# Kernel optimization log

Hardware: AMD Instinct MI355X
Metric: run time of the kernel (lower is better)

## Reference

```python
import jax, jax.numpy as jnp
import numpy as np

B, S, D = 8, 1024, 512
H, DH, OUT = 8, 64, 512
EPS = 1e-6

def _ln(x, scale, bias):
    m = jnp.mean(x, -1, keepdims=True)
    v = jnp.mean(jnp.square(x - m), -1, keepdims=True)
    return (x - m) * jax.lax.rsqrt(v + EPS) * scale + bias

def _rel_shift(x):
    # TransformerXL relative shift: [B,H,Q,P] -> [B,H,Q,P]
    b, h, q, p = x.shape
    x = jnp.pad(x, ((0, 0), (0, 0), (0, 0), (1, 0)))
    x = x.reshape(b, h, p + 1, q)
    return x[:, :, 1:, :].reshape(b, h, q, p)

def _gate(x, y, wry, wrx, wzy, wzx, why, whx, bg):
    # GTrXL GRU-style gating
    r = jax.nn.sigmoid(y @ wry + x @ wrx)
    z = jax.nn.sigmoid(y @ wzy + x @ wzx - bg)
    h = jnp.tanh(y @ why + (r * x) @ whx)
    return (1 - z) * x + z * h

def setup_inputs() -> dict:
    key = jax.random.key(0)
    ks = jax.random.split(key, 40)
    w = lambda k, shp: (0.02 * jax.random.normal(k, shp, jnp.float32))
    inp = {
        'values_keys': jax.random.normal(ks[0], (B, S, D), jnp.float32),
        'queries': jax.random.normal(ks[1], (B, S, D), jnp.float32),
        'pos_embed': jax.random.normal(ks[2], (S, D), jnp.float32),
        'mask': jnp.tril(jnp.ones((S, S), bool))[None, None],
        'ln1_scale': jnp.ones((D,), jnp.float32), 'ln1_bias': jnp.zeros((D,), jnp.float32),
        'wq': w(ks[3], (D, H, DH)), 'bq': jnp.zeros((H, DH), jnp.float32),
        'wk': w(ks[4], (D, H, DH)), 'bk': jnp.zeros((H, DH), jnp.float32),
        'wv': w(ks[5], (D, H, DH)), 'bv': jnp.zeros((H, DH), jnp.float32),
        'wr': w(ks[6], (D, H, DH)),
        'u_bias': w(ks[7], (H, DH)), 'v_bias': w(ks[8], (H, DH)),
        'wo': w(ks[9], (H, DH, OUT)), 'bo': jnp.zeros((OUT,), jnp.float32),
        'ln2_scale': jnp.ones((OUT,), jnp.float32), 'ln2_bias': jnp.zeros((OUT,), jnp.float32),
        'w1': w(ks[10], (OUT, OUT)), 'b1': jnp.zeros((OUT,), jnp.float32),
        'w2': w(ks[11], (OUT, OUT)), 'b2': jnp.zeros((OUT,), jnp.float32),
    }
    for gi, base in ((1, 12), (2, 19)):
        for j, nm in enumerate(['wry', 'wrx', 'wzy', 'wzx', 'why', 'whx']):
            inp['g%d_%s' % (gi, nm)] = w(ks[base + j], (OUT, OUT))
        inp['g%d_bg' % gi] = 2.0 * jnp.ones((OUT,), jnp.float32)
    return inp

def reference(values_keys, queries, pos_embed, mask, ln1_scale, ln1_bias, wq, bq, wk, bk, wv, bv, wr, u_bias, v_bias, wo, bo, ln2_scale, ln2_bias, w1, b1, w2, b2, g1_wry, g1_wrx, g1_wzy, g1_wzx, g1_why, g1_whx, g1_bg, g2_wry, g2_wrx, g2_wzy, g2_wzx, g2_why, g2_whx, g2_bg):
    vk = _ln(values_keys, ln1_scale, ln1_bias)
    qn = _ln(queries, ln1_scale, ln1_bias)
    q = jnp.einsum('bsd,dhk->bshk', qn, wq) + bq
    k = jnp.einsum('bsd,dhk->bshk', vk, wk) + bk
    v = jnp.einsum('bsd,dhk->bshk', vk, wv) + bv
    r = jnp.einsum('pd,dhk->phk', pos_embed, wr)
    ac = jnp.einsum('bqhk,bshk->bhqs', q + u_bias, k)
    bd = _rel_shift(jnp.einsum('bqhk,phk->bhqp', q + v_bias, r))
    scores = (ac + bd) * jnp.float32(1.0 / np.sqrt(DH))
    scores = jnp.where(mask, scores, jnp.float32(-1e9))
    attn = jax.nn.softmax(scores, axis=-1)
    o = jnp.einsum('bhqs,bshk->bqhk', attn, v)
    attn_out = jnp.einsum('bqhk,hko->bqo', o, wo) + bo
    out_attention = _gate(queries, jax.nn.relu(attn_out), g1_wry, g1_wrx, g1_wzy, g1_wzx, g1_why, g1_whx, g1_bg)
    h = _ln(out_attention, ln2_scale, ln2_bias)
    h = jax.nn.gelu(h @ w1 + b1) @ w2 + b2
    return _gate(h, jax.nn.relu(out_attention), g2_wry, g2_wrx, g2_wzy, g2_wzx, g2_why, g2_whx, g2_bg)
```

## Files before the change

kernel.cpp:

```cpp
#include <hip/hip_runtime.h>
#include <hip/hip_bf16.h>
#include <math.h>

#define TPB 256
#define B_   8
#define S_   1024
#define D_   512
#define H_   8
#define DH_  64
#define MTOK (B_ * S_)
#define NEL  (MTOK * D_)
#define WMAT (D_ * D_)

typedef __attribute__((ext_vector_type(8))) short bf8;
typedef __attribute__((ext_vector_type(4))) float f4;

__device__ __forceinline__ float ld_any(const void* p, long i, bool bf) {
  if (bf) {
    unsigned u = (unsigned)((const unsigned short*)p)[i];
    union { unsigned u; float f; } c; c.u = u << 16;
    return c.f;
  }
  return ((const float*)p)[i];
}

__device__ __forceinline__ unsigned short f2bf(float f) {
  union { float f; unsigned u; } c; c.f = f;
  unsigned u = c.u;
  u += 0x7FFFu + ((u >> 16) & 1u);
  return (unsigned short)(u >> 16);
}

typedef const void __attribute__((address_space(1)))* gp_t;
typedef void __attribute__((address_space(3)))* lp_t;
__device__ __forceinline__ void gl16(const void* g, void* l) {
  __builtin_amdgcn_global_load_lds((gp_t)(uintptr_t)g,
                                   (lp_t)(unsigned)(uintptr_t)l, 16, 0, 0);
}

struct P19 { const void* p[19]; };
struct P14 { const void* p[14]; };

__device__ __forceinline__ void ln_row(const void* src, unsigned short* dst,
                                       long row, const void* scale,
                                       const void* bias, bool bf_s, bool bf_p,
                                       int t, float* red) {
  long base = row * 512;
  float a = ld_any(src, base + t, bf_s), b = ld_any(src, base + t + 256, bf_s);
  red[t] = a + b;
  __syncthreads();
  for (int s = 128; s > 0; s >>= 1) { if (t < s) red[t] += red[t + s]; __syncthreads(); }
  float m = red[0] * (1.0f / 512.0f);
  __syncthreads();
  float da = a - m, db = b - m;
  red[t] = da * da + db * db;
  __syncthreads();
  for (int s = 128; s > 0; s >>= 1) { if (t < s) red[t] += red[t + s]; __syncthreads(); }
  float inv = rsqrtf(red[0] * (1.0f / 512.0f) + 1e-6f);
  dst[base + t] = f2bf(da * inv * ld_any(scale, t, bf_p) + ld_any(bias, t, bf_p));
  dst[base + t + 256] =
      f2bf(db * inv * ld_any(scale, t + 256, bf_p) + ld_any(bias, t + 256, bf_p));
}

__global__ __launch_bounds__(TPB) void k_prep(
    const void* __restrict__ vk_src, const void* __restrict__ q_src,
    const void* __restrict__ pos_src, const void* __restrict__ sc_src,
    const void* __restrict__ bi_src, P19 pw, P14 pp,
    unsigned short* __restrict__ vk_b, unsigned short* __restrict__ qn_b,
    float* __restrict__ qF, unsigned short* __restrict__ qB,
    unsigned short* __restrict__ posB, float* __restrict__ Pb,
    unsigned short* __restrict__ Wt, const unsigned* __restrict__ flagp) {
  __shared__ float smem[64 * 65];
  const bool bf = (*flagp == 0x3F803F80u);
  const int bx = blockIdx.x, t = threadIdx.x;
  if (bx < 16384) {
    long row = bx;
    const void* src = vk_src; unsigned short* dst = vk_b;
    if (row >= MTOK) { src = q_src; dst = qn_b; row -= MTOK; }
    ln_row(src, dst, row, sc_src, bi_src, bf, bf, t, smem);
  } else if (bx < 34844) {
    int bid = bx - 16384;
    if (bid < 16384) {
      long i = (long)bid * TPB + t;
      float v = ld_any(q_src, i, bf);
      qF[i] = v; qB[i] = f2bf(v);
    } else if (bid < 18432) {
      long i = (long)(bid - 16384) * TPB + t;
      posB[i] = f2bf(ld_any(pos_src, i, bf));
    } else {
      int i = (bid - 18432) * TPB + t;
      Pb[i] = ld_any(pp.p[i >> 9], i & 511, bf);
    }
  } else {
    int zz = bx - 34844;
    int z = zz >> 6, tile = zz & 63;
    int k0 = (tile >> 3) * 64, n0 = (tile & 7) * 64;
    const void* src = pw.p[z];
    unsigned short* dst = Wt + (size_t)z * WMAT;
#pragma unroll
    for (int i = 0; i < 16; i++) {
      int fl = i * TPB + t;
      int r = fl >> 6, c = fl & 63;
      smem[r * 65 + c] = ld_any(src, (long)(k0 + r) * 512 + n0 + c, bf);
    }
    __syncthreads();
#pragma unroll
    for (int i = 0; i < 16; i++) {
      int fl = i * TPB + t;
      int r = fl >> 6, c = fl & 63;
      dst[(size_t)(n0 + r) * 512 + k0 + c] = f2bf(smem[c * 65 + r]);
    }
  }
}

__global__ __launch_bounds__(TPB) void k_ln_bf(const void* __restrict__ src,
                                               unsigned short* __restrict__ dst,
                                               const float* __restrict__ scale,
                                               const float* __restrict__ bias) {
  __shared__ float red[TPB];
  ln_row(src, dst, blockIdx.x, scale, bias, false, false, threadIdx.x, red);
}

__device__ __forceinline__ void gemm_core(
    unsigned short* As, unsigned short* Bs,
    const unsigned short* __restrict__ A1, const unsigned short* __restrict__ W1,
    const unsigned short* __restrict__ A2, const unsigned short* __restrict__ W2,
    const float* __restrict__ bias, const float* __restrict__ xb,
    const float* __restrict__ zb, const float* __restrict__ aux1,
    const float* __restrict__ aux2,
    float* __restrict__ outF, unsigned short* __restrict__ outB,
    unsigned short* __restrict__ outB2,
    const unsigned* __restrict__ flagp, int ACT, int bm, int bn) {
  const int tid = threadIdx.x;
  const int w = tid >> 6, lane = tid & 63;
  const int quad = lane >> 4, col = lane & 15;
  const int lrow = lane >> 3;
  const int lkc  = (lane & 7) ^ lrow;
  const int sw_base = col & 7;

  f4 acc[2][2];
#pragma unroll
  for (int mi = 0; mi < 2; mi++)
#pragma unroll
    for (int ni = 0; ni < 2; ni++) acc[mi][ni] = (f4){0.f, 0.f, 0.f, 0.f};

  for (int prod = 0; prod < 2; ++prod) {
    const unsigned short* Ap = prod ? A2 : A1;
    const unsigned short* Wp = prod ? W2 : W1;
    if (!Ap) break;
    for (int k0 = 0; k0 < 512; k0 += 64) {
      __syncthreads();
      gl16(Ap + (size_t)(bm + w * 8 + lrow) * 512 + k0 + lkc * 8,
           (char*)As + w * 1024);
      const unsigned short* bS = Wp + (size_t)(bn + w * 8 + lrow) * 512 + k0 + lkc * 8;
      gl16(bS,                    (char*)Bs + w * 1024);
      gl16(bS + (size_t)32 * 512, (char*)Bs + 4096 + w * 1024);
      gl16(bS + (size_t)64 * 512, (char*)Bs + 8192 + w * 1024);
      gl16(bS + (size_t)96 * 512, (char*)Bs + 12288 + w * 1024);
      __syncthreads();
#pragma unroll
      for (int kk = 0; kk < 2; ++kk) {
        const int swz = (kk * 4 + quad) ^ sw_base;
        bf8 af[2], bfg[2];
#pragma unroll
        for (int mi = 0; mi < 2; mi++)
          af[mi] = *(const bf8*)&As[((mi * 16 + col) * 8 + swz) * 8];
#pragma unroll
        for (int ni = 0; ni < 2; ni++)
          bfg[ni] = *(const bf8*)&Bs[((w * 32 + ni * 16 + col) * 8 + swz) * 8];
#pragma unroll
        for (int mi = 0; mi < 2; mi++)
#pragma unroll
          for (int ni = 0; ni < 2; ni++)
            acc[mi][ni] = __builtin_amdgcn_mfma_f32_16x16x32_bf16(af[mi], bfg[ni],
                                                                  acc[mi][ni], 0, 0, 0);
      }
    }
  }

  const bool bfout = flagp && (*flagp == 0x3F803F80u);
#pragma unroll
  for (int mi = 0; mi < 2; mi++)
#pragma unroll
    for (int ni = 0; ni < 2; ni++) {
      const int n = bn + w * 32 + ni * 16 + col;
      const float bn_v = bias ? bias[n] : 0.f;
      const int m0 = bm + mi * 16 + quad * 4;
      if (ACT == 11 && n >= 512) {
        unsigned long long pk = 0;
#pragma unroll
        for (int r = 0; r < 4; r++) {
          float v = acc[mi][ni][r] + bn_v;
          pk |= (unsigned long long)f2bf(v) << (16 * r);
        }
        size_t dst = ((size_t)(m0 >> 10) * 512 + (n - 512)) * 1024 + (m0 & 1023);
        *(unsigned long long*)&outB2[dst] = pk;
      } else {
#pragma unroll
        for (int r = 0; r < 4; r++) {
          size_t idx = (size_t)(m0 + r) * 512 + n;
          float v = acc[mi][ni][r] + bn_v;
          if (ACT == 0) {
            if (outF) outF[idx] = v;
            if (outB) outB[idx] = f2bf(v);
          } else if (ACT == 1) {
            outB[idx] = f2bf(fmaxf(v, 0.f));
          } else if (ACT == 5) {
            float z = zb[idx], x = xb[idx];
            float g = (1.f - z) * x + z * tanhf(v);
            outF[idx] = g;
            outB[idx] = f2bf(fmaxf(g, 0.f));
          } else if (ACT == 6) {
            float t = 0.7978845608028654f * (v + 0.044715f * v * v * v);
            outB[idx] = f2bf(0.5f * v * (1.f + tanhf(t)));
          } else if (ACT == 7) {
            float z = zb[idx], x = xb[idx];
            float g = (1.f - z) * x + z * tanhf(v);
            if (bfout) outB[idx] = f2bf(g);
            else       outF[idx] = g;
          } else if (ACT == 8) {
            outB[idx]  = f2bf(v + aux1[n]);
            outB2[idx] = f2bf(v + aux2[n]);
          } else if (ACT == 10) {
            if (n < 512) {
              outB[idx] = f2bf(xb[idx] / (1.f + __expf(-v)));
            } else {
              size_t zi = (size_t)(m0 + r) * 512 + (n - 512);
              outF[zi] = 1.f / (1.f + __expf(-(v - aux1[n - 512])));
            }
          } else if (ACT == 11) {
            outB[idx] = f2bf(v);
          }
        }
      }
    }
}

__global__ __launch_bounds__(TPB) void k_gemm(
    const unsigned short* __restrict__ A1, const unsigned short* __restrict__ W1,
    const unsigned short* __restrict__ A2, const unsigned short* __restrict__ W2,
    const float* __restrict__ bias, const float* __restrict__ xb,
    const float* __restrict__ zb, const float* __restrict__ aux1,
    const float* __restrict__ aux2,
    float* __restrict__ outF, unsigned short* __restrict__ outB,
    unsigned short* __restrict__ outB2,
    const unsigned* __restrict__ flagp, int ACT) {
  __shared__ unsigned short As[32 * 64];
  __shared__ unsigned short Bs[128 * 64];
  gemm_core(As, Bs, A1, W1, A2, W2, bias, xb, zb, aux1, aux2,
            outF, outB, outB2, flagp, ACT,
            blockIdx.x * 32, blockIdx.y * 128);
}

__global__ __launch_bounds__(TPB) void k_proj(
    const unsigned short* __restrict__ qn_b, const unsigned short* __restrict__ vk_b,
    const unsigned short* __restrict__ pos_b, const unsigned short* __restrict__ Wt,
    const float* __restrict__ Pb,
    unsigned short* __restrict__ qu_b, unsigned short* __restrict__ qv_b,
    unsigned short* __restrict__ k_b, unsigned short* __restrict__ vT,
    unsigned short* __restrict__ r_b) {
  __shared__ unsigned short As[32 * 64];
  __shared__ unsigned short Bs[128 * 64];
  const int bx = blockIdx.x;
  if (bx < 1024) {
    int bm = (bx & 255) * 32, bn = (bx >> 8) * 128;
    gemm_core(As, Bs, qn_b, Wt, nullptr, nullptr, Pb + 1024, nullptr, nullptr,
              Pb + 2560, Pb + 3072, nullptr, qu_b, qv_b, nullptr, 8, bm, bn);
  } else if (bx < 3072) {
    int t = bx - 1024;
    int bm = (t & 255) * 32, bn = (t >> 8) * 128;
    gemm_core(As, Bs, vk_b, Wt + (size_t)1 * WMAT, nullptr, nullptr, Pb + 1536,
              nullptr, nullptr, nullptr, nullptr, nullptr, k_b, vT, nullptr,
              11, bm, bn);
  } else {
    int t = bx - 3072;
    int bm = (t & 31) * 32, bn = (t >> 5) * 128;
    gemm_core(As, Bs, pos_b, Wt + (size_t)3 * WMAT, nullptr, nullptr, nullptr,
              nullptr, nullptr, nullptr, nullptr, nullptr, r_b, nullptr,
              nullptr, 0, bm, bn);
  }
}

#define AC_STR 68
#define BD_STR 68

__global__ __launch_bounds__(64, 2) void k_attn6(
    const unsigned short* __restrict__ quB, const unsigned short* __restrict__ qvB,
    const unsigned short* __restrict__ kB, const unsigned short* __restrict__ vT,
    const unsigned short* __restrict__ rB, unsigned short* __restrict__ oB) {
  __shared__ float acS[16 * AC_STR];
  __shared__ float bdS[16 * BD_STR];
  const int lane = threadIdx.x;
  const int quad = lane >> 4, col = lane & 15;
  const int bx = blockIdx.x;
  const int bh = (bx & 7) * 8 + ((bx >> 3) & 7);
  const int qt = 63 - (bx >> 6);
  const int b = bh >> 3, h = bh & 7, dbase = h * 64;
  const int q0 = qt << 4;
  const int np = (qt >> 2) + 1;
  const int j0base = 1008 - q0;

  bf8 aqu[2], aqv[2];
  {
    const unsigned short* p1 = quB + (size_t)(b * 1024 + q0 + col) * 512 + dbase + quad * 8;
    const unsigned short* p2 = qvB + (size_t)(b * 1024 + q0 + col) * 512 + dbase + quad * 8;
    aqu[0] = *(const bf8*)p1; aqu[1] = *(const bf8*)(p1 + 32);
    aqv[0] = *(const bf8*)p2; aqv[1] = *(const bf8*)(p2 + 32);
  }
  f4 accO[4];
#pragma unroll
  for (int nd = 0; nd < 4; nd++) accO[nd] = (f4){0.f, 0.f, 0.f, 0.f};
  float lsum = 0.f;

  bf8 kreg[2][4], rreg[2][5], vreg[2][4];

  auto loadKR = [&](int pt) {
    const int p0 = pt << 6;
    const int j0 = j0base + p0;
#pragma unroll
    for (int ks = 0; ks < 2; ++ks) {
      const int dof = dbase + ks * 32 + quad * 8;
#pragma unroll
      for (int ni = 0; ni < 4; ++ni)
        kreg[ks][ni] =
            *(const bf8*)&kB[(size_t)(b * 1024 + p0 + ni * 16 + col) * 512 + dof];
#pragma unroll
      for (int nj = 0; nj < 5; ++nj) {
        int j = j0 + nj * 16 + col; if (j > 1023) j = 1023;
        rreg[ks][nj] = *(const bf8*)&rB[(size_t)j * 512 + dof];
      }
    }
  };
  auto loadV = [&](int pt) {
    const int p0 = pt << 6;
#pragma unroll
    for (int ks = 0; ks < 2; ++ks)
#pragma unroll
      for (int nd = 0; nd < 4; ++nd)
        vreg[ks][nd] = *(const bf8*)&vT[(size_t)(bh * 64 + nd * 16 + col) * 1024 +
                                        p0 + ks * 32 + quad * 8];
  };

  loadKR(0);
  loadV(0);
  __builtin_amdgcn_sched_barrier(0);

#pragma unroll 1
  for (int pt = 0; pt < np; ++pt) {
    const int p0 = pt << 6;

    f4 ac[4], bd[5];
#pragma unroll
    for (int ni = 0; ni < 4; ni++) ac[ni] = (f4){0.f, 0.f, 0.f, 0.f};
#pragma unroll
    for (int nj = 0; nj < 5; nj++) bd[nj] = (f4){0.f, 0.f, 0.f, 0.f};
#pragma unroll
    for (int ks = 0; ks < 2; ++ks) {
#pragma unroll
      for (int ni = 0; ni < 4; ++ni)
        ac[ni] = __builtin_amdgcn_mfma_f32_16x16x32_bf16(aqu[ks], kreg[ks][ni],
                                                         ac[ni], 0, 0, 0);
#pragma unroll
      for (int nj = 0; nj < 5; ++nj)
        bd[nj] = __builtin_amdgcn_mfma_f32_16x16x32_bf16(aqv[ks], rreg[ks][nj],
                                                         bd[nj], 0, 0, 0);
    }
    __builtin_amdgcn_sched_barrier(0);

    if (pt + 1 < np) loadKR(pt + 1);
    __builtin_amdgcn_sched_barrier(0);

#pragma unroll
    for (int ni = 0; ni < 4; ++ni)
#pragma unroll
      for (int r = 0; r < 4; ++r)
        acS[(quad * 4 + r) * AC_STR + ni * 16 + col] = ac[ni][r];
#pragma unroll
    for (int nj = 0; nj < 5; ++nj)
#pragma unroll
      for (int r = 0; r < 4; ++r) {
        int row = quad * 4 + r;
        int idx = nj * 16 + col + row - 15;
        if ((unsigned)idx < 64u) bdS[row * BD_STR + idx] = bd[nj][r];
      }
    __asm__ volatile("s_waitcnt lgkmcnt(0)" ::: "memory");

    bf8 apf[2];
    const int qg = q0 + col;
#pragma unroll
    for (int ks = 0; ks < 2; ++ks) {
      const int po = ks * 32 + quad * 8;
      f4 A0 = *(const f4*)&acS[col * AC_STR + po];
      f4 A1 = *(const f4*)&acS[col * AC_STR + po + 4];
      f4 B0 = *(const f4*)&bdS[col * BD_STR + po];
      f4 B1 = *(const f4*)&bdS[col * BD_STR + po + 4];
      const int pb = p0 + po;
      union { bf8 v; unsigned short s[8]; } ap;
#pragma unroll
      for (int jj = 0; jj < 4; ++jj) {
        float e0 = (pb + jj <= qg) ? __expf((A0[jj] + B0[jj]) * 0.125f) : 0.f;
        float e1 = (pb + 4 + jj <= qg) ? __expf((A1[jj] + B1[jj]) * 0.125f) : 0.f;
        lsum += e0 + e1;
        ap.s[jj] = f2bf(e0); ap.s[4 + jj] = f2bf(e1);
      }
      apf[ks] = ap.v;
    }

#pragma unroll
    for (int ks = 0; ks < 2; ++ks) {
#pragma unroll
      for (int nd = 0; nd < 4; ++nd)
        accO[nd] = __builtin_amdgcn_mfma_f32_16x16x32_bf16(apf[ks], vreg[ks][nd],
                                                           accO[nd], 0, 0, 0);
    }
    __builtin_amdgcn_sched_barrier(0);

    if (pt + 1 < np) loadV(pt + 1);
    __builtin_amdgcn_sched_barrier(0);
  }

  float ls = lsum;
  ls += __shfl_xor(ls, 16, 64);
  ls += __shfl_xor(ls, 32, 64);
  float lr[4];
#pragma unroll
  for (int r = 0; r < 4; ++r) lr[r] = __shfl(ls, quad * 4 + r, 64);
#pragma unroll
  for (int nd = 0; nd < 4; ++nd)
#pragma unroll
    for (int r = 0; r < 4; ++r) {
      float o = accO[nd][r] / lr[r];
      oB[(size_t)(b * 1024 + q0 + quad * 4 + r) * 512 + dbase + nd * 16 + col] = f2bf(o);
    }
}

extern "C" void kernel_launch(void* const* d_in, const int* in_sizes, int n_in,
                              void* d_out, int out_size, void* d_ws, size_t ws_size,
                              hipStream_t stream) {
  (void)in_sizes; (void)n_in; (void)out_size; (void)ws_size;
  const unsigned* flagp = (const unsigned*)d_in[4];
  char* ws = (char*)d_ws;
  const size_t MB = 1u << 20;
  auto SH = [&](int i) { return (unsigned short*)(ws + (size_t)i * 8 * MB); };

  unsigned short* vk_b = SH(0);
  unsigned short* qn_b = SH(1);
  unsigned short* qu_b = SH(2);
  unsigned short* qv_b = SH(3);
  unsigned short* k_b  = SH(4);
  unsigned short* qr_b = SH(5);
  unsigned short* vT   = SH(6);
  unsigned short* posr = SH(7);
  float* qF = (float*)(ws + 64 * MB);
  float* z1 = (float*)(ws + 80 * MB);
  float* oa = (float*)(ws + 96 * MB);
  unsigned short* Wt = (unsigned short*)(ws + 112 * MB);
  float* Pb = (float*)(ws + 122 * MB);

  unsigned short* pos_b = posr;
  unsigned short* r_b   = posr + 524288;
  unsigned short* o_b = qn_b;  unsigned short* y1 = vk_b;
  unsigned short* rx1 = qu_b;  unsigned short* y2 = qv_b;
  unsigned short* ln2h = k_b;  unsigned short* hg = qr_b;
  unsigned short* h_b = vT;    unsigned short* rx2 = posr;
  float* hF = qF;              float* z2 = z1;

  auto W = [&](int i) { return Wt + (size_t)i * WMAT; };
  dim3 bt(TPB);
  dim3 gG(MTOK / 32, 4);
  dim3 gG2(MTOK / 32, 8);

  P19 pw; const int wi[19] = {6, 8, 10, 12, 15, 19, 21,
                              23, 25, 24, 26, 27, 28, 30, 32, 31, 33, 34, 35};
  for (int i = 0; i < 19; i++) pw.p[i] = d_in[wi[i]];
  P14 pp; const int pi[14] = {4, 5, 7, 9, 11, 13, 14, 16, 17, 18, 20, 22, 29, 36};
  for (int i = 0; i < 14; i++) pp.p[i] = d_in[pi[i]];

  k_prep<<<dim3(36060), bt, 0, stream>>>(d_in[0], d_in[1], d_in[2], d_in[4],
                                         d_in[5], pw, pp, vk_b, qn_b, qF, qr_b,
                                         pos_b, Pb, Wt, flagp);

  k_proj<<<dim3(3200), bt, 0, stream>>>(qn_b, vk_b, pos_b, Wt, Pb,
                                        qu_b, qv_b, k_b, vT, r_b);

  k_attn6<<<dim3(4096), dim3(64), 0, stream>>>(qu_b, qv_b, k_b, vT, r_b, o_b);

  k_gemm<<<gG, bt, 0, stream>>>(o_b, W(4), nullptr, nullptr, Pb + 3584, nullptr,
                                nullptr, nullptr, nullptr, nullptr, y1, nullptr,
                                nullptr, 1);
  k_gemm<<<gG2, bt, 0, stream>>>(y1, W(7), qr_b, W(9), nullptr, qF, nullptr,
                                 Pb + 6144, nullptr, z1, rx1, nullptr,
                                 nullptr, 10);
  k_gemm<<<gG, bt, 0, stream>>>(y1, W(11), rx1, W(12), nullptr, qF, z1,
                                nullptr, nullptr, oa, y2, nullptr, nullptr, 5);

  k_ln_bf<<<dim3(MTOK), bt, 0, stream>>>(oa, ln2h, Pb + 4096, Pb + 4608);
  k_gemm<<<gG, bt, 0, stream>>>(ln2h, W(5), nullptr, nullptr, Pb + 5120, nullptr,
                                nullptr, nullptr, nullptr, nullptr, hg, nullptr,
                                nullptr, 6);
  k_gemm<<<gG, bt, 0, stream>>>(hg, W(6), nullptr, nullptr, Pb + 5632, nullptr,
                                nullptr, nullptr, nullptr, hF, h_b, nullptr,
                                nullptr, 0);

  k_gemm<<<gG2, bt, 0, stream>>>(y2, W(13), h_b, W(15), nullptr, hF, nullptr,
                                 Pb + 6656, nullptr, z2, rx2, nullptr,
                                 nullptr, 10);
  k_gemm<<<gG, bt, 0, stream>>>(y2, W(17), rx2, W(18), nullptr, hF, z2,
                                nullptr, nullptr, (float*)d_out,
                                (unsigned short*)d_out, nullptr, flagp, 7);
}
```

Measured before the change: 498.7 us.

## Pre-pack K, V and R into MFMA fragment order for coalesced attention loads

Adds a repacking kernel that rewrites K, transposed V and the relative-position R into a layout where each wave's MFMA operand fragment is one contiguous 1 KB block. The attention kernel then reads fragments with fully coalesced per-lane loads instead of strided 16-byte gathers across rows. Launch bounds are raised to allow more waves per SIMD. The cost is an extra kernel launch and a full read and write of K, V and R through memory, and the workspace regions it reuses must not alias live data.

```diff
diff --git a/kernel.cpp b/kernel.cpp
--- a/kernel.cpp
+++ b/kernel.cpp
@@ -119,6 +119,34 @@
                                                const float* __restrict__ bias) {
   __shared__ float red[TPB];
   ln_row(src, dst, blockIdx.x, scale, bias, false, false, threadIdx.x, red);
+}
+
+__global__ __launch_bounds__(TPB) void k_frag(
+    const unsigned short* __restrict__ kB, const unsigned short* __restrict__ vTB,
+    const unsigned short* __restrict__ rB, unsigned short* __restrict__ KF,
+    unsigned short* __restrict__ VF, unsigned short* __restrict__ RF) {
+  int c = blockIdx.x * TPB + threadIdx.x;
+  if (c < 524288) {
+    int col = c & 15, quad = (c >> 4) & 3, ks = (c >> 6) & 1, h = (c >> 7) & 7;
+    int pg = (c >> 10) & 63, b = c >> 16;
+    bf8 v = *(const bf8*)&kB[(size_t)(b * 1024 + pg * 16 + col) * 512 +
+                             h * 64 + ks * 32 + quad * 8];
+    *(bf8*)&KF[(size_t)c * 8] = v;
+  } else if (c < 1048576) {
+    int d = c - 524288;
+    int col = d & 15, quad = (d >> 4) & 3, nd = (d >> 6) & 3, ks = (d >> 8) & 1;
+    int pt = (d >> 9) & 15, h = (d >> 13) & 7, b = d >> 16;
+    bf8 v = *(const bf8*)&vTB[(size_t)((b * 8 + h) * 64 + nd * 16 + col) * 1024 +
+                              pt * 64 + ks * 32 + quad * 8];
+    *(bf8*)&VF[(size_t)d * 8] = v;
+  } else {
+    int d = c - 1048576;
+    int col = d & 15, quad = (d >> 4) & 3, ks = (d >> 6) & 1, g = (d >> 7) & 63;
+    int h = d >> 13;
+    bf8 v = *(const bf8*)&rB[(size_t)(g * 16 + col) * 512 +
+                             h * 64 + ks * 32 + quad * 8];
+    *(bf8*)&RF[(size_t)d * 8] = v;
+  }
 }
 
 __device__ __forceinline__ void gemm_core(
@@ -284,10 +312,10 @@
 #define AC_STR 68
 #define BD_STR 68
 
-__global__ __launch_bounds__(64, 2) void k_attn6(
+__global__ __launch_bounds__(64, 4) void k_attn7(
     const unsigned short* __restrict__ quB, const unsigned short* __restrict__ qvB,
-    const unsigned short* __restrict__ kB, const unsigned short* __restrict__ vT,
-    const unsigned short* __restrict__ rB, unsigned short* __restrict__ oB) {
+    const unsigned short* __restrict__ KF, const unsigned short* __restrict__ VF,
+    const unsigned short* __restrict__ RF, unsigned short* __restrict__ oB) {
   __shared__ float acS[16 * AC_STR];
   __shared__ float bdS[16 * BD_STR];
   const int lane = threadIdx.x;
@@ -298,7 +326,6 @@
   const int b = bh >> 3, h = bh & 7, dbase = h * 64;
   const int q0 = qt << 4;
   const int np = (qt >> 2) + 1;
-  const int j0base = 1008 - q0;
 
   bf8 aqu[2], aqv[2];
   {
@@ -315,30 +342,31 @@
   bf8 kreg[2][4], rreg[2][5], vreg[2][4];
 
   auto loadKR = [&](int pt) {
-    const int p0 = pt << 6;
-    const int j0 = j0base + p0;
+    const int pg = pt * 4;
+    const int g0 = 63 - qt + pt * 4;
 #pragma unroll
     for (int ks = 0; ks < 2; ++ks) {
-      const int dof = dbase + ks * 32 + quad * 8;
-#pragma unroll
-      for (int ni = 0; ni < 4; ++ni)
-        kreg[ks][ni] =
-            *(const bf8*)&kB[(size_t)(b * 1024 + p0 + ni * 16 + col) * 512 + dof];
+#pragma unroll
+      for (int ni = 0; ni < 4; ++ni) {
+        size_t kidx = ((((size_t)b * 64 + pg + ni) * 8 + h) * 2 + ks) * 64 + lane;
+        kreg[ks][ni] = *(const bf8*)&KF[kidx * 8];
+      }
 #pragma unroll
       for (int nj = 0; nj < 5; ++nj) {
-        int j = j0 + nj * 16 + col; if (j > 1023) j = 1023;
-        rreg[ks][nj] = *(const bf8*)&rB[(size_t)j * 512 + dof];
+        int g = g0 + nj; if (g > 63) g = 63;
+        size_t ridx = (((size_t)h * 64 + g) * 2 + ks) * 64 + lane;
+        rreg[ks][nj] = *(const bf8*)&RF[ridx * 8];
       }
     }
   };
   auto loadV = [&](int pt) {
-    const int p0 = pt << 6;
 #pragma unroll
     for (int ks = 0; ks < 2; ++ks)
 #pragma unroll
-      for (int nd = 0; nd < 4; ++nd)
-        vreg[ks][nd] = *(const bf8*)&vT[(size_t)(bh * 64 + nd * 16 + col) * 1024 +
-                                        p0 + ks * 32 + quad * 8];
+      for (int nd = 0; nd < 4; ++nd) {
+        size_t vidx = (((((size_t)b * 8 + h) * 16 + pt) * 2 + ks) * 4 + nd) * 64 + lane;
+        vreg[ks][nd] = *(const bf8*)&VF[vidx * 8];
+      }
   };
 
   loadKR(0);
@@ -457,6 +485,10 @@
   unsigned short* Wt = (unsigned short*)(ws + 112 * MB);
   float* Pb = (float*)(ws + 122 * MB);
 
+  unsigned short* KF = (unsigned short*)(ws + 80 * MB);
+  unsigned short* RF = (unsigned short*)(ws + 88 * MB);
+  unsigned short* VF = (unsigned short*)(ws + 96 * MB);
+
   unsigned short* pos_b = posr;
   unsigned short* r_b   = posr + 524288;
   unsigned short* o_b = qn_b;  unsigned short* y1 = vk_b;
@@ -483,7 +515,9 @@
   k_proj<<<dim3(3200), bt, 0, stream>>>(qn_b, vk_b, pos_b, Wt, Pb,
                                         qu_b, qv_b, k_b, vT, r_b);
 
-  k_attn6<<<dim3(4096), dim3(64), 0, stream>>>(qu_b, qv_b, k_b, vT, r_b, o_b);
+  k_frag<<<dim3(4352), bt, 0, stream>>>(k_b, vT, r_b, KF, VF, RF);
+
+  k_attn7<<<dim3(4096), dim3(64), 0, stream>>>(qu_b, qv_b, KF, VF, RF, o_b);
 
   k_gemm<<<gG, bt, 0, stream>>>(o_b, W(4), nullptr, nullptr, Pb + 3584, nullptr,
                                 nullptr, nullptr, nullptr, nullptr, y1, nullptr,
```

Result: slower. 671.1 us (+34.6%).
